# Performance work log

Measured on AMD Instinct MI355X. Metric: run time of the kernel, lower is better.

The kernel has to match this reference:

```python
import jax, jax.numpy as jnp
import numpy as np

BN_EPS = 1e-5


def _lin(key, fan_in, fan_out):
    k1, k2 = jax.random.split(key)
    s = 1.0 / np.sqrt(fan_in)
    w = jax.random.uniform(k1, (fan_in, fan_out), jnp.float32, -s, s)
    b = jax.random.uniform(k2, (fan_out,), jnp.float32, -s, s)
    return w, b


def setup_inputs() -> dict:
    key = jax.random.key(0)
    ks = jax.random.split(key, 24)
    N, E, F_IN, E_DIM, G = 50000, 800000, 64, 16, 128
    inp = {}
    inp["x"] = jax.random.normal(ks[0], (N, F_IN), jnp.float32)
    inp["edge_attr"] = jax.random.normal(ks[1], (E, E_DIM), jnp.float32)
    inp["edge_index"] = jax.random.randint(ks[2], (2, E), 0, N, jnp.int64)
    inp["batch_ids"] = jnp.sort(jax.random.randint(ks[3], (N,), 0, G, jnp.int64))
    # conv1: edge lin (16->64), mlp 64->256->256
    inp["we1"], inp["be1"] = _lin(ks[4], E_DIM, F_IN)
    inp["w1a"], inp["b1a"] = _lin(ks[5], F_IN, 256)
    inp["w1b"], inp["b1b"] = _lin(ks[6], 256, 256)
    inp["bn1_g"] = jnp.ones((256,), jnp.float32)
    inp["bn1_b"] = jnp.zeros((256,), jnp.float32)
    inp["bn1_m"] = 0.1 * jax.random.normal(ks[7], (256,), jnp.float32)
    inp["bn1_v"] = jnp.abs(jax.random.normal(ks[8], (256,), jnp.float32)) + 0.5
    # conv2: edge lin (16->256), mlp 256->128->128
    inp["we2"], inp["be2"] = _lin(ks[9], E_DIM, 256)
    inp["w2a"], inp["b2a"] = _lin(ks[10], 256, 128)
    inp["w2b"], inp["b2b"] = _lin(ks[11], 128, 128)
    inp["bn2_g"] = jnp.ones((128,), jnp.float32)
    inp["bn2_b"] = jnp.zeros((128,), jnp.float32)
    inp["bn2_m"] = 0.1 * jax.random.normal(ks[12], (128,), jnp.float32)
    inp["bn2_v"] = jnp.abs(jax.random.normal(ks[13], (128,), jnp.float32)) + 0.5
    # conv3: edge lin (16->128), mlp 128->64->64
    inp["we3"], inp["be3"] = _lin(ks[14], E_DIM, 128)
    inp["w3a"], inp["b3a"] = _lin(ks[15], 128, 64)
    inp["w3b"], inp["b3b"] = _lin(ks[16], 64, 64)
    inp["bn3_g"] = jnp.ones((64,), jnp.float32)
    inp["bn3_b"] = jnp.zeros((64,), jnp.float32)
    inp["bn3_m"] = 0.1 * jax.random.normal(ks[17], (64,), jnp.float32)
    inp["bn3_v"] = jnp.abs(jax.random.normal(ks[18], (64,), jnp.float32)) + 0.5
    inp["fc1_w"], inp["fc1_b"] = _lin(ks[19], 64, 16)
    inp["fc2_w"], inp["fc2_b"] = _lin(ks[20], 16, 1)
    return inp


def _gine(x, edge_index, edge_attr, we, be, wa, ba, wb, bb):
    # GINEConv, eps=0: mlp(x + sum_j relu(x_j + lin_e(e_ji)))
    src, dst = edge_index[0], edge_index[1]
    msg = jax.nn.relu(x[src] + edge_attr @ we + be)  # [E, d]
    agg = jax.ops.segment_sum(msg, dst, num_segments=x.shape[0])
    h = x + agg
    return jax.nn.relu(h @ wa + ba) @ wb + bb


def _bn(x, g, b, m, v):
    return (x - m) * jax.lax.rsqrt(v + BN_EPS) * g + b


def reference(x, edge_attr, edge_index, batch_ids,
              we1, be1, w1a, b1a, w1b, b1b, bn1_g, bn1_b, bn1_m, bn1_v,
              we2, be2, w2a, b2a, w2b, b2b, bn2_g, bn2_b, bn2_m, bn2_v,
              we3, be3, w3a, b3a, w3b, b3b, bn3_g, bn3_b, bn3_m, bn3_v,
              fc1_w, fc1_b, fc2_w, fc2_b):
    G = 128  # num graphs
    h = _gine(x, edge_index, edge_attr, we1, be1, w1a, b1a, w1b, b1b)
    h = _bn(jax.nn.relu(h), bn1_g, bn1_b, bn1_m, bn1_v)
    h = _gine(h, edge_index, edge_attr, we2, be2, w2a, b2a, w2b, b2b)
    h = _bn(jax.nn.relu(h), bn2_g, bn2_b, bn2_m, bn2_v)
    h = _gine(h, edge_index, edge_attr, we3, be3, w3a, b3a, w3b, b3b)
    h = _bn(jax.nn.relu(h), bn3_g, bn3_b, bn3_m, bn3_v)
    pooled = jax.ops.segment_sum(h, batch_ids, num_segments=G)  # [G, 64]
    out = jax.nn.relu(pooled @ fc1_w + fc1_b) @ fc2_w + fc2_b  # [G, 1]
    return out
```

## Files before the change

### kernel.cpp

```cpp
#include <hip/hip_runtime.h>
#include <hip/hip_bf16.h>

#define BN_EPS 1e-5f

typedef __attribute__((ext_vector_type(8))) short short8v;
typedef __attribute__((ext_vector_type(4))) float f32x4;
typedef _Float16 f16x2 __attribute__((ext_vector_type(2)));
typedef __hip_bfloat16 bf16;
typedef unsigned short ushort_t;
typedef unsigned int uint_t;

__global__ void count_kernel(const int* __restrict__ dst, int* __restrict__ deg,
                             int E, int N) {
    int i = blockIdx.x * blockDim.x + threadIdx.x;
    if (i >= E) return;
    int d = dst[i];
    d = min(max(d, 0), N - 1);
    atomicAdd(&deg[d], 1);
}

__global__ __launch_bounds__(256) void scan1_kernel(const int* __restrict__ deg,
                                                    int* __restrict__ bsum, int N) {
    int t = threadIdx.x, b = blockIdx.x;
    int i = b * 256 + t;
    int v = (i < N) ? deg[i] : 0;
#pragma unroll
    for (int d = 32; d; d >>= 1) v += __shfl_xor(v, d, 64);
    __shared__ int ws[4];
    if ((t & 63) == 0) ws[t >> 6] = v;
    __syncthreads();
    if (t == 0) bsum[b] = ws[0] + ws[1] + ws[2] + ws[3];
}

__global__ __launch_bounds__(256) void scan2_kernel(int* __restrict__ bsum, int nb) {
    int t = threadIdx.x;
    int v = (t < nb) ? bsum[t] : 0;
    int lane = t & 63, w = t >> 6;
    int inc = v;
#pragma unroll
    for (int d = 1; d < 64; d <<= 1) {
        int u = __shfl_up(inc, d, 64);
        if (lane >= d) inc += u;
    }
    __shared__ int ws[4];
    if (lane == 63) ws[w] = inc;
    __syncthreads();
    int base = 0;
    for (int j = 0; j < w; ++j) base += ws[j];
    if (t < nb) bsum[t] = base + inc - v;
}

__global__ __launch_bounds__(256) void scan3_kernel(const int* __restrict__ deg,
                                                    const int* __restrict__ bsum,
                                                    int* __restrict__ off,
                                                    int* __restrict__ cur, int N) {
    int t = threadIdx.x, b = blockIdx.x;
    int i = b * 256 + t;
    int v = (i < N) ? deg[i] : 0;
    int lane = t & 63, w = t >> 6;
    int inc = v;
#pragma unroll
    for (int d = 1; d < 64; d <<= 1) {
        int u = __shfl_up(inc, d, 64);
        if (lane >= d) inc += u;
    }
    __shared__ int ws[4];
    if (lane == 63) ws[w] = inc;
    __syncthreads();
    int base = bsum[b];
    for (int j = 0; j < w; ++j) base += ws[j];
    int excl = base + inc - v;
    if (i < N) { off[i] = excl; cur[i] = excl; }
    if (i == N - 1) off[N] = excl + v;
}

__global__ void fill_kernel(const int* __restrict__ src, const int* __restrict__ dst,
                            const float* __restrict__ ea, int* __restrict__ cur,
                            int* __restrict__ srcs, uint_t* __restrict__ each,
                            int E, int N) {
    int i = blockIdx.x * blockDim.x + threadIdx.x;
    if (i >= E) return;
    int d = dst[i];
    d = min(max(d, 0), N - 1);
    int p = atomicAdd(&cur[d], 1);
    srcs[p] = min(max(src[i], 0), N - 1);
    uint_t pk[8];
#pragma unroll
    for (int q = 0; q < 4; ++q) {
        float4 a = *(const float4*)&ea[(size_t)i * 16 + q * 4];
        f16x2 h0 = {(_Float16)a.x, (_Float16)a.y};
        f16x2 h1 = {(_Float16)a.z, (_Float16)a.w};
        pk[q * 2 + 0] = __builtin_bit_cast(uint_t, h0);
        pk[q * 2 + 1] = __builtin_bit_cast(uint_t, h1);
    }
    *(uint4*)&each[(size_t)p * 8 + 0] = *(uint4*)&pk[0];
    *(uint4*)&each[(size_t)p * 8 + 4] = *(uint4*)&pk[4];
}

__global__ void conv_bf16_kernel(const float* __restrict__ in, bf16* __restrict__ out,
                                 int n) {
    int i = (blockIdx.x * blockDim.x + threadIdx.x) * 4;
    if (i + 3 < n) {
        float4 v = *(const float4*)&in[i];
        out[i + 0] = __float2bfloat16(v.x);
        out[i + 1] = __float2bfloat16(v.y);
        out[i + 2] = __float2bfloat16(v.z);
        out[i + 3] = __float2bfloat16(v.w);
    } else {
        for (int j = i; j < n && j >= 0; ++j) out[j] = __float2bfloat16(in[j]);
    }
}

__global__ void conv_w_kernel(const float* __restrict__ w1a, const float* __restrict__ w1b,
                              const float* __restrict__ w2a, const float* __restrict__ w2b,
                              const float* __restrict__ w3a, const float* __restrict__ w3b,
                              bf16* __restrict__ wt) {
    int t = blockIdx.x * blockDim.x + threadIdx.x;
    const float* w; int K, N, base, r;
    if (t < 16384)       { w = w1a; K = 64;  N = 256; base = 0;      r = t; }
    else if (t < 81920)  { w = w1b; K = 256; N = 256; base = 16384;  r = t - 16384; }
    else if (t < 114688) { w = w2a; K = 256; N = 128; base = 81920;  r = t - 81920; }
    else if (t < 131072) { w = w2b; K = 128; N = 128; base = 114688; r = t - 114688; }
    else if (t < 139264) { w = w3a; K = 128; N = 64;  base = 131072; r = t - 131072; }
    else if (t < 143360) { w = w3b; K = 64;  N = 64;  base = 139264; r = t - 139264; }
    else return;
    int k = r % K, n = r / K;
    wt[base + r] = __float2bfloat16(w[(size_t)k * N + n]);
}

__global__ void conv_wef_kernel(const float* __restrict__ we1, const float* __restrict__ we2,
                                const float* __restrict__ we3, uint_t* __restrict__ wef) {
    int t = blockIdx.x * blockDim.x + threadIdx.x;
    const float* w; int D, base, r;
    if (t < 512)        { w = we1; D = 64;  base = 0;    r = t; }
    else if (t < 2560)  { w = we2; D = 256; base = 512;  r = t - 512; }
    else if (t < 3584)  { w = we3; D = 128; base = 2560; r = t - 2560; }
    else return;
    int p = r / D, col = r % D;
    f16x2 h = {(_Float16)w[(size_t)(2 * p) * D + col],
               (_Float16)w[(size_t)(2 * p + 1) * D + col]};
    wef[base + r] = __builtin_bit_cast(uint_t, h);
}

template <int C>
__global__ __launch_bounds__(256) void msg_fused(
    const uint_t* __restrict__ each, const int* __restrict__ srcs,
    const int* __restrict__ off, const bf16* __restrict__ x,
    const uint_t* __restrict__ wef, const float* __restrict__ be,
    bf16* __restrict__ t, int N) {
    constexpr int D = C * 64;
    const int lane = threadIdx.x & 63;
    const int n = blockIdx.x * 4 + (threadIdx.x >> 6);
    if (n >= N) return;
    const int col0 = lane * C;

    uint_t wreg[8][C];
#pragma unroll
    for (int p = 0; p < 8; ++p)
#pragma unroll
        for (int c = 0; c < C; ++c) wreg[p][c] = wef[p * D + col0 + c];
    float breg[C];
#pragma unroll
    for (int c = 0; c < C; ++c) breg[c] = be[col0 + c];

    float acc[C];
#pragma unroll
    for (int c = 0; c < C; ++c) acc[c] = 0.f;

    const ushort_t* xp = (const ushort_t*)x;

    const int i0 = __builtin_amdgcn_readfirstlane(off[n]);
    const int i1 = __builtin_amdgcn_readfirstlane(off[n + 1]);

#define BF2F(u) (__builtin_bit_cast(float, (unsigned)(u) << 16))
#define H2(u) (__builtin_bit_cast(f16x2, u))

    int i = i0;
    for (; i + 4 <= i1; i += 4) {
        int s[4];
#pragma unroll
        for (int j = 0; j < 4; ++j) s[j] = __builtin_amdgcn_readfirstlane(srcs[i + j]);
        ushort_t xv[4][C];
#pragma unroll
        for (int j = 0; j < 4; ++j) {
            if constexpr (C == 4) {
                *(ushort4*)xv[j] = *(const ushort4*)&xp[(size_t)s[j] * D + col0];
            } else if constexpr (C == 2) {
                *(ushort2*)xv[j] = *(const ushort2*)&xp[(size_t)s[j] * D + col0];
            } else {
                xv[j][0] = xp[(size_t)s[j] * D + col0];
            }
        }
        uint_t e[4][8];
#pragma unroll
        for (int j = 0; j < 4; ++j)
#pragma unroll
            for (int p = 0; p < 8; ++p) e[j][p] = each[(size_t)(i + j) * 8 + p];

        float m[4][C];
#pragma unroll
        for (int j = 0; j < 4; ++j)
#pragma unroll
            for (int c = 0; c < C; ++c)
                m[j][c] = __builtin_amdgcn_fdot2(H2(e[j][0]), H2(wreg[0][c]), breg[c], false);
#pragma unroll
        for (int p = 1; p < 8; ++p)
#pragma unroll
            for (int j = 0; j < 4; ++j)
#pragma unroll
                for (int c = 0; c < C; ++c)
                    m[j][c] = __builtin_amdgcn_fdot2(H2(e[j][p]), H2(wreg[p][c]), m[j][c], false);
#pragma unroll
        for (int j = 0; j < 4; ++j)
#pragma unroll
            for (int c = 0; c < C; ++c)
                acc[c] += fmaxf(m[j][c] + BF2F(xv[j][c]), 0.f);
    }
    for (; i < i1; ++i) {
        const int s0 = __builtin_amdgcn_readfirstlane(srcs[i]);
        ushort_t xv0[C];
        if constexpr (C == 4) {
            *(ushort4*)xv0 = *(const ushort4*)&xp[(size_t)s0 * D + col0];
        } else if constexpr (C == 2) {
            *(ushort2*)xv0 = *(const ushort2*)&xp[(size_t)s0 * D + col0];
        } else {
            xv0[0] = xp[(size_t)s0 * D + col0];
        }
        uint_t e0[8];
#pragma unroll
        for (int p = 0; p < 8; ++p) e0[p] = each[(size_t)i * 8 + p];
        float m0[C];
#pragma unroll
        for (int c = 0; c < C; ++c)
            m0[c] = __builtin_amdgcn_fdot2(H2(e0[0]), H2(wreg[0][c]), breg[c], false);
#pragma unroll
        for (int p = 1; p < 8; ++p)
#pragma unroll
            for (int c = 0; c < C; ++c)
                m0[c] = __builtin_amdgcn_fdot2(H2(e0[p]), H2(wreg[p][c]), m0[c], false);
#pragma unroll
        for (int c = 0; c < C; ++c) acc[c] += fmaxf(m0[c] + BF2F(xv0[c]), 0.f);
    }

#pragma unroll
    for (int c = 0; c < C; ++c) {
        float xo = BF2F(xp[(size_t)n * D + col0 + c]);
        t[(size_t)n * D + col0 + c] = __float2bfloat16(xo + acc[c]);
    }
#undef BF2F
#undef H2
}

template <int NCOLS>
__global__ __launch_bounds__(256) void gemm_mfma(
    const bf16* __restrict__ A, const bf16* __restrict__ Wt,
    const float* __restrict__ bias, const float* __restrict__ bng,
    const float* __restrict__ bnb, const float* __restrict__ bnm,
    const float* __restrict__ bnv, bf16* __restrict__ C,
    const int* __restrict__ batch, float* __restrict__ pooled,
    int M, int K, int mode) {
    constexpr int NT = NCOLS / 16;
    const int lane = threadIdx.x & 63;
    const int w = threadIdx.x >> 6;
    const int mbase = blockIdx.x * 128 + w * 32;
    const int r16 = lane & 15;
    const int kg = lane >> 4;

    f32x4 acc[2][NT];
#pragma unroll
    for (int f = 0; f < 2; ++f)
#pragma unroll
        for (int nt = 0; nt < NT; ++nt) acc[f][nt] = (f32x4){0.f, 0.f, 0.f, 0.f};

    const short* Ap = (const short*)A;
    const short* Wp = (const short*)Wt;

    for (int k0 = 0; k0 < K; k0 += 32) {
        short8v a0 = *(const short8v*)&Ap[(size_t)(mbase + r16) * K + k0 + kg * 8];
        short8v a1 = *(const short8v*)&Ap[(size_t)(mbase + 16 + r16) * K + k0 + kg * 8];
#pragma unroll
        for (int nt = 0; nt < NT; ++nt) {
            short8v b = *(const short8v*)&Wp[(size_t)(nt * 16 + r16) * K + k0 + kg * 8];
            acc[0][nt] = __builtin_amdgcn_mfma_f32_16x16x32_bf16(a0, b, acc[0][nt], 0, 0, 0);
            acc[1][nt] = __builtin_amdgcn_mfma_f32_16x16x32_bf16(a1, b, acc[1][nt], 0, 0, 0);
        }
    }

    float bs[NT], sc[NT], sh[NT];
#pragma unroll
    for (int nt = 0; nt < NT; ++nt) {
        int col = nt * 16 + r16;
        bs[nt] = bias[col];
        sc[nt] = 1.f; sh[nt] = 0.f;
        if (mode >= 2) {
            sc[nt] = rsqrtf(bnv[col] + BN_EPS) * bng[col];
            sh[nt] = bnb[col] - bnm[col] * sc[nt];
        }
    }

#pragma unroll
    for (int f = 0; f < 2; ++f) {
#pragma unroll
        for (int rg = 0; rg < 4; ++rg) {
            int row = mbase + f * 16 + kg * 4 + rg;
            if (row >= M) continue;
            int g = 0;
            if (mode == 3) g = min(max(batch[row], 0), 127);
#pragma unroll
            for (int nt = 0; nt < NT; ++nt) {
                int col = nt * 16 + r16;
                float z = acc[f][nt][rg] + bs[nt];
                z = fmaxf(z, 0.f);
                if (mode >= 2) z = z * sc[nt] + sh[nt];
                if (mode == 3)
                    atomicAdd(&pooled[g * NCOLS + col], z);
                else
                    C[(size_t)row * NCOLS + col] = __float2bfloat16(z);
            }
        }
    }
}

__global__ __launch_bounds__(128) void head_kernel(
    const float* __restrict__ pooled, const float* __restrict__ w1,
    const float* __restrict__ b1, const float* __restrict__ w2,
    const float* __restrict__ b2, float* __restrict__ out) {
    const int g = threadIdx.x;
    float p[64];
#pragma unroll
    for (int i = 0; i < 64; ++i) p[i] = pooled[g * 64 + i];
    float o = b2[0];
#pragma unroll
    for (int j = 0; j < 16; ++j) {
        float hsum = b1[j];
#pragma unroll
        for (int i = 0; i < 64; ++i) hsum = fmaf(p[i], w1[i * 16 + j], hsum);
        o = fmaf(fmaxf(hsum, 0.f), w2[j], o);
    }
    out[g] = o;
}

extern "C" void kernel_launch(void* const* d_in, const int* in_sizes, int n_in,
                              void* d_out, int out_size, void* d_ws,
                              size_t ws_size, hipStream_t stream) {
    const float* x     = (const float*)d_in[0];
    const float* ea    = (const float*)d_in[1];
    const int*   ei    = (const int*)d_in[2];
    const int*   batch = (const int*)d_in[3];
    const float* we1 = (const float*)d_in[4];
    const float* be1 = (const float*)d_in[5];
    const float* w1a = (const float*)d_in[6];
    const float* b1a = (const float*)d_in[7];
    const float* w1b = (const float*)d_in[8];
    const float* b1b = (const float*)d_in[9];
    const float* bn1g = (const float*)d_in[10];
    const float* bn1b = (const float*)d_in[11];
    const float* bn1m = (const float*)d_in[12];
    const float* bn1v = (const float*)d_in[13];
    const float* we2 = (const float*)d_in[14];
    const float* be2 = (const float*)d_in[15];
    const float* w2a = (const float*)d_in[16];
    const float* b2a = (const float*)d_in[17];
    const float* w2b = (const float*)d_in[18];
    const float* b2b = (const float*)d_in[19];
    const float* bn2g = (const float*)d_in[20];
    const float* bn2b = (const float*)d_in[21];
    const float* bn2m = (const float*)d_in[22];
    const float* bn2v = (const float*)d_in[23];
    const float* we3 = (const float*)d_in[24];
    const float* be3 = (const float*)d_in[25];
    const float* w3a = (const float*)d_in[26];
    const float* b3a = (const float*)d_in[27];
    const float* w3b = (const float*)d_in[28];
    const float* b3b = (const float*)d_in[29];
    const float* bn3g = (const float*)d_in[30];
    const float* bn3b = (const float*)d_in[31];
    const float* bn3m = (const float*)d_in[32];
    const float* bn3v = (const float*)d_in[33];
    const float* fc1w = (const float*)d_in[34];
    const float* fc1b = (const float*)d_in[35];
    const float* fc2w = (const float*)d_in[36];
    const float* fc2b = (const float*)d_in[37];

    const int N = in_sizes[0] / 64;
    const int E = in_sizes[1] / 16;
    const int M_pad = ((N + 127) / 128) * 128;
    const int* src = ei;
    const int* dst = ei + E;

    char* wsp = (char*)d_ws;
    auto alloc = [&](size_t bytes) -> void* {
        void* p = (void*)wsp;
        wsp += (bytes + 255) & ~(size_t)255;
        return p;
    };
    const int nb = (N + 255) / 256;
    int* deg    = (int*)alloc((size_t)N * 4);
    int* off    = (int*)alloc((size_t)(N + 1) * 4);
    int* cur    = (int*)alloc((size_t)N * 4);
    int* bsum   = (int*)alloc((size_t)nb * 4);
    int* srcs   = (int*)alloc((size_t)E * 4);
    uint_t* each = (uint_t*)alloc((size_t)E * 8 * 4);
    bf16* xb    = (bf16*)alloc((size_t)N * 64 * 2);
    bf16* tb    = (bf16*)alloc((size_t)M_pad * 256 * 2);
    bf16* ub    = (bf16*)alloc((size_t)M_pad * 256 * 2);
    bf16* hb    = (bf16*)alloc((size_t)M_pad * 256 * 2);
    bf16* wt    = (bf16*)alloc((size_t)143360 * 2);
    uint_t* wef = (uint_t*)alloc((size_t)3584 * 4);
    float* pooled = (float*)alloc(128 * 64 * 4);

    bf16* wt1a = wt + 0;
    bf16* wt1b = wt + 16384;
    bf16* wt2a = wt + 81920;
    bf16* wt2b = wt + 114688;
    bf16* wt3a = wt + 131072;
    bf16* wt3b = wt + 139264;
    uint_t* wef1 = wef + 0;
    uint_t* wef2 = wef + 512;
    uint_t* wef3 = wef + 2560;

    hipMemsetAsync(deg, 0, (size_t)N * 4, stream);
    hipMemsetAsync(pooled, 0, 128 * 64 * 4, stream);

    conv_bf16_kernel<<<(N * 64 / 4 + 255) / 256, 256, 0, stream>>>(x, xb, N * 64);
    conv_w_kernel<<<(143360 + 255) / 256, 256, 0, stream>>>(w1a, w1b, w2a, w2b,
                                                            w3a, w3b, wt);
    conv_wef_kernel<<<(3584 + 255) / 256, 256, 0, stream>>>(we1, we2, we3, wef);

    int eb = (E + 255) / 256;
    count_kernel<<<eb, 256, 0, stream>>>(dst, deg, E, N);
    scan1_kernel<<<nb, 256, 0, stream>>>(deg, bsum, N);
    scan2_kernel<<<1, 256, 0, stream>>>(bsum, nb);
    scan3_kernel<<<nb, 256, 0, stream>>>(deg, bsum, off, cur, N);
    fill_kernel<<<eb, 256, 0, stream>>>(src, dst, ea, cur, srcs, each, E, N);

    const int gblk = M_pad / 128;
    const int mblk = (N + 3) / 4;

    msg_fused<1><<<mblk, 256, 0, stream>>>(each, srcs, off, xb, wef1, be1, tb, N);
    gemm_mfma<256><<<gblk, 256, 0, stream>>>(tb, wt1a, b1a, nullptr, nullptr, nullptr,
                                             nullptr, ub, nullptr, nullptr, N, 64, 1);
    gemm_mfma<256><<<gblk, 256, 0, stream>>>(ub, wt1b, b1b, bn1g, bn1b, bn1m, bn1v,
                                             hb, nullptr, nullptr, N, 256, 2);
    msg_fused<4><<<mblk, 256, 0, stream>>>(each, srcs, off, hb, wef2, be2, tb, N);
    gemm_mfma<128><<<gblk, 256, 0, stream>>>(tb, wt2a, b2a, nullptr, nullptr, nullptr,
                                             nullptr, ub, nullptr, nullptr, N, 256, 1);
    gemm_mfma<128><<<gblk, 256, 0, stream>>>(ub, wt2b, b2b, bn2g, bn2b, bn2m, bn2v,
                                             hb, nullptr, nullptr, N, 128, 2);
    msg_fused<2><<<mblk, 256, 0, stream>>>(each, srcs, off, hb, wef3, be3, tb, N);
    gemm_mfma<64><<<gblk, 256, 0, stream>>>(tb, wt3a, b3a, nullptr, nullptr, nullptr,
                                            nullptr, ub, nullptr, nullptr, N, 128, 1);
    gemm_mfma<64><<<gblk, 256, 0, stream>>>(ub, wt3b, b3b, bn3g, bn3b, bn3m, bn3v,
                                            nullptr, batch, pooled, N, 64, 3);

    head_kernel<<<1, 128, 0, stream>>>(pooled, fc1w, fc1b, fc2w, fc2b, (float*)d_out);
}
```

Baseline: 490.8 us.

## Fuse MLP GEMM pairs via LDS, merge setup kernels, fold scan passes, prefetch sources

Each GINE MLP's two GEMMs are fused into one kernel that keeps the hidden activation in LDS, so the intermediate bf16 buffer is never written to or read from global memory. The conversion kernels and memsets are merged into a single launch. The middle scan pass is folded into the final scan, where each block sums the preceding block totals itself. The message kernel also prefetches the next four source indices one iteration ahead. Together these reduce launch count and global traffic, at the cost of large LDS use (about 66KB for H=256), which may lower occupancy.

```diff
diff --git a/kernel.cpp b/kernel.cpp
--- a/kernel.cpp
+++ b/kernel.cpp
@@ -32,10 +32,25 @@
     if (t == 0) bsum[b] = ws[0] + ws[1] + ws[2] + ws[3];
 }
 
-__global__ __launch_bounds__(256) void scan2_kernel(int* __restrict__ bsum, int nb) {
-    int t = threadIdx.x;
-    int v = (t < nb) ? bsum[t] : 0;
+__global__ __launch_bounds__(256) void scan3_kernel(const int* __restrict__ deg,
+                                                    const int* __restrict__ bsum,
+                                                    int* __restrict__ off,
+                                                    int* __restrict__ cur,
+                                                    int N, int nb) {
+    int t = threadIdx.x, b = blockIdx.x;
     int lane = t & 63, w = t >> 6;
+
+    int partial = 0;
+    for (int j = t; j < b; j += 256) partial += bsum[j];
+#pragma unroll
+    for (int d = 32; d; d >>= 1) partial += __shfl_xor(partial, d, 64);
+    __shared__ int bsm[4];
+    if (lane == 0) bsm[w] = partial;
+    __syncthreads();
+    int base = bsm[0] + bsm[1] + bsm[2] + bsm[3];
+
+    int i = b * 256 + t;
+    int v = (i < N) ? deg[i] : 0;
     int inc = v;
 #pragma unroll
     for (int d = 1; d < 64; d <<= 1) {
@@ -45,29 +60,6 @@
     __shared__ int ws[4];
     if (lane == 63) ws[w] = inc;
     __syncthreads();
-    int base = 0;
-    for (int j = 0; j < w; ++j) base += ws[j];
-    if (t < nb) bsum[t] = base + inc - v;
-}
-
-__global__ __launch_bounds__(256) void scan3_kernel(const int* __restrict__ deg,
-                                                    const int* __restrict__ bsum,
-                                                    int* __restrict__ off,
-                                                    int* __restrict__ cur, int N) {
-    int t = threadIdx.x, b = blockIdx.x;
-    int i = b * 256 + t;
-    int v = (i < N) ? deg[i] : 0;
-    int lane = t & 63, w = t >> 6;
-    int inc = v;
-#pragma unroll
-    for (int d = 1; d < 64; d <<= 1) {
-        int u = __shfl_up(inc, d, 64);
-        if (lane >= d) inc += u;
-    }
-    __shared__ int ws[4];
-    if (lane == 63) ws[w] = inc;
-    __syncthreads();
-    int base = bsum[b];
     for (int j = 0; j < w; ++j) base += ws[j];
     int excl = base + inc - v;
     if (i < N) { off[i] = excl; cur[i] = excl; }
@@ -97,49 +89,65 @@
     *(uint4*)&each[(size_t)p * 8 + 4] = *(uint4*)&pk[4];
 }
 
-__global__ void conv_bf16_kernel(const float* __restrict__ in, bf16* __restrict__ out,
-                                 int n) {
-    int i = (blockIdx.x * blockDim.x + threadIdx.x) * 4;
-    if (i + 3 < n) {
-        float4 v = *(const float4*)&in[i];
-        out[i + 0] = __float2bfloat16(v.x);
-        out[i + 1] = __float2bfloat16(v.y);
-        out[i + 2] = __float2bfloat16(v.z);
-        out[i + 3] = __float2bfloat16(v.w);
-    } else {
-        for (int j = i; j < n && j >= 0; ++j) out[j] = __float2bfloat16(in[j]);
-    }
-}
-
-__global__ void conv_w_kernel(const float* __restrict__ w1a, const float* __restrict__ w1b,
-                              const float* __restrict__ w2a, const float* __restrict__ w2b,
-                              const float* __restrict__ w3a, const float* __restrict__ w3b,
-                              bf16* __restrict__ wt) {
+__global__ void megaconv_kernel(
+    const float* __restrict__ x, bf16* __restrict__ xb, int nx4,
+    const float* __restrict__ w1a, const float* __restrict__ w1b,
+    const float* __restrict__ w2a, const float* __restrict__ w2b,
+    const float* __restrict__ w3a, const float* __restrict__ w3b,
+    bf16* __restrict__ wt,
+    const float* __restrict__ we1, const float* __restrict__ we2,
+    const float* __restrict__ we3, uint_t* __restrict__ wef,
+    int* __restrict__ deg, int N, float* __restrict__ pooled) {
     int t = blockIdx.x * blockDim.x + threadIdx.x;
-    const float* w; int K, N, base, r;
-    if (t < 16384)       { w = w1a; K = 64;  N = 256; base = 0;      r = t; }
-    else if (t < 81920)  { w = w1b; K = 256; N = 256; base = 16384;  r = t - 16384; }
-    else if (t < 114688) { w = w2a; K = 256; N = 128; base = 81920;  r = t - 81920; }
-    else if (t < 131072) { w = w2b; K = 128; N = 128; base = 114688; r = t - 114688; }
-    else if (t < 139264) { w = w3a; K = 128; N = 64;  base = 131072; r = t - 131072; }
-    else if (t < 143360) { w = w3b; K = 64;  N = 64;  base = 139264; r = t - 139264; }
-    else return;
-    int k = r % K, n = r / K;
-    wt[base + r] = __float2bfloat16(w[(size_t)k * N + n]);
-}
-
-__global__ void conv_wef_kernel(const float* __restrict__ we1, const float* __restrict__ we2,
-                                const float* __restrict__ we3, uint_t* __restrict__ wef) {
-    int t = blockIdx.x * blockDim.x + threadIdx.x;
-    const float* w; int D, base, r;
-    if (t < 512)        { w = we1; D = 64;  base = 0;    r = t; }
-    else if (t < 2560)  { w = we2; D = 256; base = 512;  r = t - 512; }
-    else if (t < 3584)  { w = we3; D = 128; base = 2560; r = t - 2560; }
-    else return;
-    int p = r / D, col = r % D;
-    f16x2 h = {(_Float16)w[(size_t)(2 * p) * D + col],
-               (_Float16)w[(size_t)(2 * p + 1) * D + col]};
-    wef[base + r] = __builtin_bit_cast(uint_t, h);
+    if (t < nx4) {
+        int i = t * 4;
+        float4 v = *(const float4*)&x[i];
+        xb[i + 0] = __float2bfloat16(v.x);
+        xb[i + 1] = __float2bfloat16(v.y);
+        xb[i + 2] = __float2bfloat16(v.z);
+        xb[i + 3] = __float2bfloat16(v.w);
+        return;
+    }
+    t -= nx4;
+    if (t < 143360) {
+        const float* w; int K, Nc, base, r;
+        if (t < 16384)       { w = w1a; K = 64;  Nc = 256; base = 0;      r = t; }
+        else if (t < 81920)  { w = w1b; K = 256; Nc = 256; base = 16384;  r = t - 16384; }
+        else if (t < 114688) { w = w2a; K = 256; Nc = 128; base = 81920;  r = t - 81920; }
+        else if (t < 131072) { w = w2b; K = 128; Nc = 128; base = 114688; r = t - 114688; }
+        else if (t < 139264) { w = w3a; K = 128; Nc = 64;  base = 131072; r = t - 131072; }
+        else                 { w = w3b; K = 64;  Nc = 64;  base = 139264; r = t - 139264; }
+        int k = r % K, n = r / K;
+        wt[base + r] = __float2bfloat16(w[(size_t)k * Nc + n]);
+        return;
+    }
+    t -= 143360;
+    if (t < 3584) {
+        const float* w; int D, base, r;
+        if (t < 512)        { w = we1; D = 64;  base = 0;    r = t; }
+        else if (t < 2560)  { w = we2; D = 256; base = 512;  r = t - 512; }
+        else                { w = we3; D = 128; base = 2560; r = t - 2560; }
+        int p = r / D, col = r % D;
+        f16x2 h = {(_Float16)w[(size_t)(2 * p) * D + col],
+                   (_Float16)w[(size_t)(2 * p + 1) * D + col]};
+        wef[base + r] = __builtin_bit_cast(uint_t, h);
+        return;
+    }
+    t -= 3584;
+    {
+        int nd4 = (N + 3) / 4;
+        if (t < nd4) {
+            int i = t * 4;
+#pragma unroll
+            for (int j = 0; j < 4; ++j)
+                if (i + j < N) deg[i + j] = 0;
+            return;
+        }
+        t -= nd4;
+        if (t < 2048) {
+            *(float4*)&pooled[t * 4] = make_float4(0.f, 0.f, 0.f, 0.f);
+        }
+    }
 }
 
 template <int C>
@@ -176,10 +184,16 @@
 #define H2(u) (__builtin_bit_cast(f16x2, u))
 
     int i = i0;
+    int sN[4] = {0, 0, 0, 0};
+    if (i + 4 <= i1) {
+#pragma unroll
+        for (int j = 0; j < 4; ++j)
+            sN[j] = __builtin_amdgcn_readfirstlane(srcs[i + j]);
+    }
     for (; i + 4 <= i1; i += 4) {
         int s[4];
 #pragma unroll
-        for (int j = 0; j < 4; ++j) s[j] = __builtin_amdgcn_readfirstlane(srcs[i + j]);
+        for (int j = 0; j < 4; ++j) s[j] = sN[j];
         ushort_t xv[4][C];
 #pragma unroll
         for (int j = 0; j < 4; ++j) {
@@ -190,6 +204,11 @@
             } else {
                 xv[j][0] = xp[(size_t)s[j] * D + col0];
             }
+        }
+        if (i + 8 <= i1) {
+#pragma unroll
+            for (int j = 0; j < 4; ++j)
+                sN[j] = __builtin_amdgcn_readfirstlane(srcs[i + 4 + j]);
         }
         uint_t e[4][8];
 #pragma unroll
@@ -251,51 +270,90 @@
 #undef H2
 }
 
-template <int NCOLS>
-__global__ __launch_bounds__(256) void gemm_mfma(
-    const bf16* __restrict__ A, const bf16* __restrict__ Wt,
-    const float* __restrict__ bias, const float* __restrict__ bng,
+template <int H, int NC>
+__global__ __launch_bounds__(256) void mlp_fused(
+    const bf16* __restrict__ A, const bf16* __restrict__ W1t,
+    const float* __restrict__ b1, const bf16* __restrict__ W2t,
+    const float* __restrict__ b2, const float* __restrict__ bng,
     const float* __restrict__ bnb, const float* __restrict__ bnm,
     const float* __restrict__ bnv, bf16* __restrict__ C,
     const int* __restrict__ batch, float* __restrict__ pooled,
-    int M, int K, int mode) {
-    constexpr int NT = NCOLS / 16;
+    int M, int K1, int mode) {
+    constexpr int NT1 = H / 16;
+    constexpr int NT2 = NC / 16;
+    constexpr int LDH = H + 8;
+    __shared__ __align__(16) ushort_t u_lds[128 * LDH];
+
     const int lane = threadIdx.x & 63;
     const int w = threadIdx.x >> 6;
-    const int mbase = blockIdx.x * 128 + w * 32;
     const int r16 = lane & 15;
     const int kg = lane >> 4;
-
-    f32x4 acc[2][NT];
+    const int mbase = blockIdx.x * 128 + w * 32;
+    const int lbase = w * 32;
+
+    const short* Ap = (const short*)A;
+    const short* W1p = (const short*)W1t;
+    const short* W2p = (const short*)W2t;
+
+    {
+        f32x4 acc[2][NT1];
+#pragma unroll
+        for (int f = 0; f < 2; ++f)
+#pragma unroll
+            for (int nt = 0; nt < NT1; ++nt) acc[f][nt] = (f32x4){0.f, 0.f, 0.f, 0.f};
+
+        for (int k0 = 0; k0 < K1; k0 += 32) {
+            short8v a0 = *(const short8v*)&Ap[(size_t)(mbase + r16) * K1 + k0 + kg * 8];
+            short8v a1 = *(const short8v*)&Ap[(size_t)(mbase + 16 + r16) * K1 + k0 + kg * 8];
+#pragma unroll
+            for (int nt = 0; nt < NT1; ++nt) {
+                short8v b = *(const short8v*)&W1p[(size_t)(nt * 16 + r16) * K1 + k0 + kg * 8];
+                acc[0][nt] = __builtin_amdgcn_mfma_f32_16x16x32_bf16(a0, b, acc[0][nt], 0, 0, 0);
+                acc[1][nt] = __builtin_amdgcn_mfma_f32_16x16x32_bf16(a1, b, acc[1][nt], 0, 0, 0);
+            }
+        }
+#pragma unroll
+        for (int nt = 0; nt < NT1; ++nt) {
+            int col = nt * 16 + r16;
+            float bs = b1[col];
+#pragma unroll
+            for (int f = 0; f < 2; ++f) {
+#pragma unroll
+                for (int rg = 0; rg < 4; ++rg) {
+                    int rl = lbase + f * 16 + kg * 4 + rg;
+                    float z = fmaxf(acc[f][nt][rg] + bs, 0.f);
+                    u_lds[rl * LDH + col] =
+                        __builtin_bit_cast(ushort_t, __float2bfloat16(z));
+                }
+            }
+        }
+    }
+    __syncthreads();
+
+    f32x4 acc2[2][NT2];
 #pragma unroll
     for (int f = 0; f < 2; ++f)
 #pragma unroll
-        for (int nt = 0; nt < NT; ++nt) acc[f][nt] = (f32x4){0.f, 0.f, 0.f, 0.f};
-
-    const short* Ap = (const short*)A;
-    const short* Wp = (const short*)Wt;
-
-    for (int k0 = 0; k0 < K; k0 += 32) {
-        short8v a0 = *(const short8v*)&Ap[(size_t)(mbase + r16) * K + k0 + kg * 8];
-        short8v a1 = *(const short8v*)&Ap[(size_t)(mbase + 16 + r16) * K + k0 + kg * 8];
-#pragma unroll
-        for (int nt = 0; nt < NT; ++nt) {
-            short8v b = *(const short8v*)&Wp[(size_t)(nt * 16 + r16) * K + k0 + kg * 8];
-            acc[0][nt] = __builtin_amdgcn_mfma_f32_16x16x32_bf16(a0, b, acc[0][nt], 0, 0, 0);
-            acc[1][nt] = __builtin_amdgcn_mfma_f32_16x16x32_bf16(a1, b, acc[1][nt], 0, 0, 0);
-        }
-    }
-
-    float bs[NT], sc[NT], sh[NT];
-#pragma unroll
-    for (int nt = 0; nt < NT; ++nt) {
+        for (int nt = 0; nt < NT2; ++nt) acc2[f][nt] = (f32x4){0.f, 0.f, 0.f, 0.f};
+
+    for (int k0 = 0; k0 < H; k0 += 32) {
+        short8v a0 = *(const short8v*)&u_lds[(lbase + r16) * LDH + k0 + kg * 8];
+        short8v a1 = *(const short8v*)&u_lds[(lbase + 16 + r16) * LDH + k0 + kg * 8];
+#pragma unroll
+        for (int nt = 0; nt < NT2; ++nt) {
+            short8v b = *(const short8v*)&W2p[(size_t)(nt * 16 + r16) * H + k0 + kg * 8];
+            acc2[0][nt] = __builtin_amdgcn_mfma_f32_16x16x32_bf16(a0, b, acc2[0][nt], 0, 0, 0);
+            acc2[1][nt] = __builtin_amdgcn_mfma_f32_16x16x32_bf16(a1, b, acc2[1][nt], 0, 0, 0);
+        }
+    }
+
+    float bs[NT2], sc[NT2], sh[NT2];
+#pragma unroll
+    for (int nt = 0; nt < NT2; ++nt) {
         int col = nt * 16 + r16;
-        bs[nt] = bias[col];
-        sc[nt] = 1.f; sh[nt] = 0.f;
-        if (mode >= 2) {
-            sc[nt] = rsqrtf(bnv[col] + BN_EPS) * bng[col];
-            sh[nt] = bnb[col] - bnm[col] * sc[nt];
-        }
+        bs[nt] = b2[col];
+        sc[nt] = rsqrtf(bnv[col] + BN_EPS) * bng[col];
+        sh[nt] = bnb[col] - bnm[col] * sc[nt];
     }
 
 #pragma unroll
@@ -307,15 +365,14 @@
             int g = 0;
             if (mode == 3) g = min(max(batch[row], 0), 127);
 #pragma unroll
-            for (int nt = 0; nt < NT; ++nt) {
+            for (int nt = 0; nt < NT2; ++nt) {
                 int col = nt * 16 + r16;
-                float z = acc[f][nt][rg] + bs[nt];
-                z = fmaxf(z, 0.f);
-                if (mode >= 2) z = z * sc[nt] + sh[nt];
+                float z = fmaxf(acc2[f][nt][rg] + bs[nt], 0.f);
+                z = z * sc[nt] + sh[nt];
                 if (mode == 3)
-                    atomicAdd(&pooled[g * NCOLS + col], z);
+                    atomicAdd(&pooled[g * NC + col], z);
                 else
-                    C[(size_t)row * NCOLS + col] = __float2bfloat16(z);
+                    C[(size_t)row * NC + col] = __float2bfloat16(z);
             }
         }
     }
@@ -403,7 +460,6 @@
     uint_t* each = (uint_t*)alloc((size_t)E * 8 * 4);
     bf16* xb    = (bf16*)alloc((size_t)N * 64 * 2);
     bf16* tb    = (bf16*)alloc((size_t)M_pad * 256 * 2);
-    bf16* ub    = (bf16*)alloc((size_t)M_pad * 256 * 2);
     bf16* hb    = (bf16*)alloc((size_t)M_pad * 256 * 2);
     bf16* wt    = (bf16*)alloc((size_t)143360 * 2);
     uint_t* wef = (uint_t*)alloc((size_t)3584 * 4);
@@ -419,39 +475,35 @@
     uint_t* wef2 = wef + 512;
     uint_t* wef3 = wef + 2560;
 
-    hipMemsetAsync(deg, 0, (size_t)N * 4, stream);
-    hipMemsetAsync(pooled, 0, 128 * 64 * 4, stream);
-
-    conv_bf16_kernel<<<(N * 64 / 4 + 255) / 256, 256, 0, stream>>>(x, xb, N * 64);
-    conv_w_kernel<<<(143360 + 255) / 256, 256, 0, stream>>>(w1a, w1b, w2a, w2b,
-                                                            w3a, w3b, wt);
-    conv_wef_kernel<<<(3584 + 255) / 256, 256, 0, stream>>>(we1, we2, we3, wef);
+    {
+        int nx4 = N * 64 / 4;
+        int total = nx4 + 143360 + 3584 + (N + 3) / 4 + 2048;
+        megaconv_kernel<<<(total + 255) / 256, 256, 0, stream>>>(
+            x, xb, nx4, w1a, w1b, w2a, w2b, w3a, w3b, wt, we1, we2, we3, wef,
+            deg, N, pooled);
+    }
 
     int eb = (E + 255) / 256;
     count_kernel<<<eb, 256, 0, stream>>>(dst, deg, E, N);
     scan1_kernel<<<nb, 256, 0, stream>>>(deg, bsum, N);
-    scan2_kernel<<<1, 256, 0, stream>>>(bsum, nb);
-    scan3_kernel<<<nb, 256, 0, stream>>>(deg, bsum, off, cur, N);
+    scan3_kernel<<<nb, 256, 0, stream>>>(deg, bsum, off, cur, N, nb);
     fill_kernel<<<eb, 256, 0, stream>>>(src, dst, ea, cur, srcs, each, E, N);
 
     const int gblk = M_pad / 128;
     const int mblk = (N + 3) / 4;
 
     msg_fused<1><<<mblk, 256, 0, stream>>>(each, srcs, off, xb, wef1, be1, tb, N);
-    gemm_mfma<256><<<gblk, 256, 0, stream>>>(tb, wt1a, b1a, nullptr, nullptr, nullptr,
-                                             nullptr, ub, nullptr, nullptr, N, 64, 1);
-    gemm_mfma<256><<<gblk, 256, 0, stream>>>(ub, wt1b, b1b, bn1g, bn1b, bn1m, bn1v,
-                                             hb, nullptr, nullptr, N, 256, 2);
+    mlp_fused<256, 256><<<gblk, 256, 0, stream>>>(tb, wt1a, b1a, wt1b, b1b,
+                                                  bn1g, bn1b, bn1m, bn1v,
+                                                  hb, nullptr, nullptr, N, 64, 2);
     msg_fused<4><<<mblk, 256, 0, stream>>>(each, srcs, off, hb, wef2, be2, tb, N);
-    gemm_mfma<128><<<gblk, 256, 0, stream>>>(tb, wt2a, b2a, nullptr, nullptr, nullptr,
-                                             nullptr, ub, nullptr, nullptr, N, 256, 1);
-    gemm_mfma<128><<<gblk, 256, 0, stream>>>(ub, wt2b, b2b, bn2g, bn2b, bn2m, bn2v,
-                                             hb, nullptr, nullptr, N, 128, 2);
+    mlp_fused<128, 128><<<gblk, 256, 0, stream>>>(tb, wt2a, b2a, wt2b, b2b,
+                                                  bn2g, bn2b, bn2m, bn2v,
+                                                  hb, nullptr, nullptr, N, 256, 2);
     msg_fused<2><<<mblk, 256, 0, stream>>>(each, srcs, off, hb, wef3, be3, tb, N);
-    gemm_mfma<64><<<gblk, 256, 0, stream>>>(tb, wt3a, b3a, nullptr, nullptr, nullptr,
-                                            nullptr, ub, nullptr, nullptr, N, 128, 1);
-    gemm_mfma<64><<<gblk, 256, 0, stream>>>(ub, wt3b, b3b, bn3g, bn3b, bn3m, bn3v,
-                                            nullptr, batch, pooled, N, 64, 3);
+    mlp_fused<64, 64><<<gblk, 256, 0, stream>>>(tb, wt3a, b3a, wt3b, b3b,
+                                                bn3g, bn3b, bn3m, bn3v,
+                                                nullptr, batch, pooled, N, 128, 3);
 
     head_kernel<<<1, 128, 0, stream>>>(pooled, fc1w, fc1b, fc2w, fc2b, (float*)d_out);
 }
```

After: 445.5 us. -9.2%, faster.
